# Optimization experiments

Measured on AMD Instinct MI355X. Metric: run time of the kernel, lower is better.

## Reference

```python
import jax, jax.numpy as jnp
import numpy as np

HIDDEN = 256
HEADS = 4
N_CHECKINS = 500000
N_POIS = 50000


def setup_inputs() -> dict:
    key = jax.random.key(0)
    ks = jax.random.split(key, 12)
    lim = 1.0 / np.sqrt(HIDDEN)
    def lin(k):
        kw, kb = jax.random.split(k)
        W = jax.random.uniform(kw, (HIDDEN, HIDDEN), jnp.float32, -lim, lim)
        b = jax.random.uniform(kb, (HIDDEN,), jnp.float32, -lim, lim)
        return W, b
    Wq, bq = lin(ks[0]); Wk, bk = lin(ks[1]); Wv, bv = lin(ks[2]); Wo, bo = lin(ks[3])
    # xavier_uniform for S [1, hidden]: gain=1, fan_in=hidden, fan_out=1
    a = np.sqrt(6.0 / (HIDDEN + 1))
    S = jax.random.uniform(ks[4], (1, HIDDEN), jnp.float32, -a, a)
    prelu_a = jnp.float32(0.25)  # PReLU default init
    x = jax.random.normal(ks[5], (N_CHECKINS, HIDDEN), jnp.float32)
    checkin_to_poi = jax.random.randint(ks[6], (N_CHECKINS,), 0, N_POIS, jnp.int64 if jax.config.jax_enable_x64 else jnp.int32)
    return {"x": x, "checkin_to_poi": checkin_to_poi, "num_pois": N_POIS,
            "Wq": Wq, "bq": bq, "Wk": Wk, "bk": bk, "Wv": Wv, "bv": bv,
            "Wo": Wo, "bo": bo, "S": S, "prelu_a": prelu_a}


def reference(x, checkin_to_poi, num_pois, Wq, bq, Wk, bk, Wv, bv, Wo, bo, S, prelu_a):
    C = x.shape[1]
    H = HEADS
    d = C // H
    idx = checkin_to_poi
    K = x @ Wk.T + bk                      # [N, C]
    V = x @ Wv.T + bv                      # [N, C]
    Q = S @ Wq.T + bq                      # [1, C]
    Ks = K.reshape(-1, H, d)
    Vs = V.reshape(-1, H, d)
    Qs = Q.reshape(1, H, d)
    scale = jnp.sqrt(jnp.float32(C))
    scores = (Ks * Qs).sum(-1) / scale     # [N, H]
    # segment softmax over POI groups (pyg_softmax)
    smax = jax.ops.segment_max(scores, idx, num_segments=num_pois)  # [P, H]
    smax = jnp.where(jnp.isfinite(smax), smax, 0.0)  # empty segments -> -inf -> 0
    e = jnp.exp(scores - smax[idx])
    denom = jax.ops.segment_sum(e, idx, num_segments=num_pois)      # [P, H]
    alpha = e / (denom[idx] + 1e-16)       # [N, H]
    weighted_V = Vs * alpha[..., None]     # [N, H, d]
    poi_agg = jax.ops.segment_sum(weighted_V.reshape(-1, C), idx, num_segments=num_pois)  # [P, C]
    O = Q + poi_agg                        # broadcast Q over POIs
    O = O + jax.nn.relu(O @ Wo.T + bo)
    O = jnp.where(O >= 0, O, prelu_a * O)  # PReLU (single shared parameter)
    return jnp.nan_to_num(O, nan=0.0)
```

## Files before the change

kernel.cpp:

```cpp
#include <hip/hip_runtime.h>
#include <stdint.h>

typedef __bf16 bf16x8 __attribute__((ext_vector_type(8)));
typedef float f32x4 __attribute__((ext_vector_type(4)));

#define MFMA16(A, B, C) __builtin_amdgcn_mfma_f32_16x16x32_bf16((A), (B), (C), 0, 0, 0)

__device__ __forceinline__ float b2f(unsigned short u) {
    union { unsigned int i; float f; } v; v.i = ((unsigned int)u) << 16; return v.f;
}
__device__ __forceinline__ unsigned short f2b(float f) {
    union { float f; unsigned int i; } v; v.f = f;
    unsigned int x = v.i;
    return (unsigned short)((x + 0x7FFFu + ((x >> 16) & 1u)) >> 16);
}
__device__ __forceinline__ float ldf(const void* p, long i, int isbf) {
    return isbf ? b2f(((const unsigned short*)p)[i]) : ((const float*)p)[i];
}

__global__ void k_probe(const unsigned int* __restrict__ wq,
                        const unsigned int* __restrict__ idxw, int* __restrict__ flags) {
    if (threadIdx.x == 0) {
        int ok = 0;
        for (int i = 0; i < 8; i++) {
            unsigned int e = (wq[i] >> 7) & 0xFFu;
            if (e >= 0x60u && e <= 0x7Cu) ok++;
        }
        flags[0] = (ok == 8) ? 1 : 0;
        int z = 0, lr = 0;
        for (int i = 0; i < 4; i++) {
            if (idxw[2 * i + 1] == 0u) z++;
            if (idxw[2 * i] < 0x4000000u) lr++;
        }
        flags[1] = (z == 4 && lr == 4) ? 1 : 0;
    }
}

__global__ void k_q(const void* __restrict__ S, const void* __restrict__ Wq,
                    const void* __restrict__ bq, const void* __restrict__ prelu,
                    const int* __restrict__ flags, float* __restrict__ Q,
                    float* __restrict__ pf) {
    int isbf = flags[0];
    int c = threadIdx.x;
    float acc = 0.f;
    for (int j = 0; j < 256; j++) acc += ldf(S, j, isbf) * ldf(Wq, (long)c * 256 + j, isbf);
    Q[c] = acc + ldf(bq, c, isbf);
    if (c == 0)
        pf[0] = isbf ? b2f(((const unsigned short*)prelu)[0]) : ((const float*)prelu)[0];
}

__global__ void k_qk(const void* __restrict__ Wk, const void* __restrict__ bk,
                     const float* __restrict__ Q, const int* __restrict__ flags,
                     unsigned short* __restrict__ qkb, float* __restrict__ qb) {
    int isbf = flags[0];
    int h = blockIdx.x, j = threadIdx.x;
    float acc = 0.f;
    if (h < 4) {
        for (int d = 0; d < 64; d++) acc += ldf(Wk, (long)(h * 64 + d) * 256 + j, isbf) * Q[h * 64 + d];
        acc *= 0.0625f;
    }
    qkb[h * 256 + j] = f2b(acc);
    if (j == 0) {
        float s = 0.f;
        if (h < 4) {
            for (int d = 0; d < 64; d++) s += ldf(bk, h * 64 + d, isbf) * Q[h * 64 + d];
            s *= 0.0625f;
        }
        qb[h] = s;
    }
}

__global__ void k_cvt(const void* __restrict__ Wv, const void* __restrict__ Wo,
                      const int* __restrict__ flags, unsigned short* __restrict__ Wvb,
                      unsigned short* __restrict__ Wob) {
    int isbf = flags[0];
    long i = (long)blockIdx.x * 256 + threadIdx.x;
    const void* src = (i < 65536) ? Wv : Wo;
    unsigned short* dst = (i < 65536) ? Wvb : Wob;
    long k = (i < 65536) ? i : i - 65536;
    dst[k] = isbf ? ((const unsigned short*)src)[k] : f2b(((const float*)src)[k]);
}

__global__ __launch_bounds__(256) void k_v(
    const void* __restrict__ x, const int* __restrict__ idxp,
    const unsigned short* __restrict__ Wvb, const unsigned short* __restrict__ qkb,
    const float* __restrict__ qb, const int* __restrict__ flags,
    float* __restrict__ denom, float* __restrict__ vagg, int N) {
    __shared__ unsigned short xs[128 * 264];
    __shared__ float es[128][4];
    int isbf = flags[0], is64 = flags[1];
    int tid = threadIdx.x;
    long base = (long)blockIdx.x * 128;

#pragma unroll
    for (int ch = 0; ch < 16; ch++) {
        int i16 = tid + ch * 256;
        int row = i16 >> 5;
        int col = (i16 & 31) * 8;
        long grow = base + row;
        uint4 t;
        if (grow < N) {
            if (isbf) {
                t = *(const uint4*)((const unsigned short*)x + grow * 256 + col);
            } else {
                const float* xp = (const float*)x + grow * 256 + col;
                float4 a = *(const float4*)xp;
                float4 b = *(const float4*)(xp + 4);
                t.x = (unsigned int)f2b(a.x) | ((unsigned int)f2b(a.y) << 16);
                t.y = (unsigned int)f2b(a.z) | ((unsigned int)f2b(a.w) << 16);
                t.z = (unsigned int)f2b(b.x) | ((unsigned int)f2b(b.y) << 16);
                t.w = (unsigned int)f2b(b.z) | ((unsigned int)f2b(b.w) << 16);
            }
        } else {
            t.x = t.y = t.z = t.w = 0u;
        }
        *(uint4*)&xs[row * 264 + col] = t;
    }
    __syncthreads();

    int w = tid >> 6, l = tid & 63;
    int m = l & 15, q = l >> 4;

    int ids[2][4];
#pragma unroll
    for (int g2 = 0; g2 < 2; g2++)
#pragma unroll
        for (int r = 0; r < 4; r++) {
            long gr = base + w * 32 + g2 * 16 + q * 4 + r;
            ids[g2][r] = (gr < N) ? (is64 ? idxp[gr << 1] : idxp[gr]) : 0;
        }

    bf16x8 a[2][8];
#pragma unroll
    for (int g2 = 0; g2 < 2; g2++)
#pragma unroll
        for (int s = 0; s < 8; s++)
            a[g2][s] = *(const bf16x8*)&xs[(w * 32 + g2 * 16 + m) * 264 + q * 8 + s * 32];

    {
        const bf16x8* qkp = (const bf16x8*)(qkb + (size_t)m * 256);
        bf16x8 qf[8];
#pragma unroll
        for (int s = 0; s < 8; s++) qf[s] = qkp[q + s * 4];
        float qbm = qb[m & 3];
#pragma unroll
        for (int g2 = 0; g2 < 2; g2++) {
            f32x4 sacc = {0.f, 0.f, 0.f, 0.f};
#pragma unroll
            for (int s = 0; s < 8; s++) sacc = MFMA16(a[g2][s], qf[s], sacc);
            if (m < 4) {
#pragma unroll
                for (int r = 0; r < 4; r++) {
                    int row = w * 32 + g2 * 16 + q * 4 + r;
                    long gr = base + row;
                    float e = 0.f;
                    if (gr < N) {
                        e = __expf(sacc[r] + qbm);
                        unsafeAtomicAdd(&denom[(long)ids[g2][r] * 4 + m], e);
                    }
                    es[row][m] = e;
                }
            }
        }
    }

#pragma unroll 1
    for (int t = 0; t < 16; t++) {
        int h_t = t >> 2;
        const bf16x8* wvp = (const bf16x8*)(Wvb + (size_t)(t * 16 + m) * 256);
        bf16x8 b[8];
#pragma unroll
        for (int s = 0; s < 8; s++) b[s] = wvp[q + s * 4];
#pragma unroll
        for (int g2 = 0; g2 < 2; g2++) {
            f32x4 acc = {0.f, 0.f, 0.f, 0.f};
#pragma unroll
            for (int s = 0; s < 8; s++) acc = MFMA16(a[g2][s], b[s], acc);
#pragma unroll
            for (int r = 0; r < 4; r++) {
                int row = w * 32 + g2 * 16 + q * 4 + r;
                long gr = base + row;
                if (gr < N) {
                    float val = acc[r] * es[row][h_t];
                    unsafeAtomicAdd(&vagg[(long)ids[g2][r] * 256 + t * 16 + m], val);
                }
            }
        }
    }
}

__global__ __launch_bounds__(256) void k_out(
    const float* __restrict__ Q, const float* __restrict__ denom,
    const float* __restrict__ vagg, const void* __restrict__ bv,
    const unsigned short* __restrict__ Wob, const void* __restrict__ bo,
    const float* __restrict__ pf, const int* __restrict__ flags,
    void* __restrict__ out, int P) {
    __shared__ float Os[4][16 * 264];
    int isbf = flags[0];
    int tid = threadIdx.x;
    int w = tid >> 6, l = tid & 63;
    int m = l & 15, q = l >> 4;
    long pbase = (long)blockIdx.x * 64 + w * 16;
    float aP = pf[0];
    long pm = pbase + m;
    bool vm = pm < P;

    float den4[4], rd4[4];
#pragma unroll
    for (int h = 0; h < 4; h++) {
        float d = vm ? denom[pm * 4 + h] : 0.f;
        den4[h] = d;
        rd4[h] = 1.0f / (d + 1e-16f);
    }

    bf16x8 of[8];
#pragma unroll
    for (int s = 0; s < 8; s++) {
        int c0 = q * 8 + s * 32;
        int h = s >> 1;
        bf16x8 ov;
        if (vm) {
            const float* ag = vagg + pm * 256 + c0;
#pragma unroll
            for (int j = 0; j < 8; j++) {
                float o = Q[c0 + j] + (ag[j] + ldf(bv, c0 + j, isbf) * den4[h]) * rd4[h];
                Os[w][m * 264 + c0 + j] = o;
                ov[j] = (__bf16)o;
            }
        } else {
#pragma unroll
            for (int j = 0; j < 8; j++) { Os[w][m * 264 + c0 + j] = 0.f; ov[j] = (__bf16)0.0f; }
        }
        of[s] = ov;
    }

#pragma unroll 1
    for (int t = 0; t < 16; t++) {
        const bf16x8* wop = (const bf16x8*)(Wob + (size_t)(t * 16 + m) * 256);
        f32x4 acc = {0.f, 0.f, 0.f, 0.f};
#pragma unroll
        for (int s = 0; s < 8; s++) acc = MFMA16(of[s], wop[q + s * 4], acc);
        int c = t * 16 + m;
        float boc = ldf(bo, c, isbf);
#pragma unroll
        for (int r = 0; r < 4; r++) {
            int row = q * 4 + r;
            long p = pbase + row;
            if (p < P) {
                float Ov = Os[w][row * 264 + c];
                float lin = fmaxf(acc[r] + boc, 0.f);
                float res = Ov + lin;
                res = (res >= 0.f) ? res : aP * res;
                if (res != res) res = 0.f;
                if (isbf) ((unsigned short*)out)[p * 256 + c] = f2b(res);
                else      ((float*)out)[p * 256 + c] = res;
            }
        }
    }
}

extern "C" void kernel_launch(void* const* d_in, const int* in_sizes, int n_in,
                              void* d_out, int out_size, void* d_ws, size_t ws_size,
                              hipStream_t stream) {
    const void* x  = d_in[0];
    const int* idx = (const int*)d_in[1];
    const void* Wq = d_in[3];
    const void* bq = d_in[4];
    const void* Wk = d_in[5];
    const void* bk = d_in[6];
    const void* Wv = d_in[7];
    const void* bv = d_in[8];
    const void* Wo = d_in[9];
    const void* bo = d_in[10];
    const void* S  = d_in[11];
    const void* pr = d_in[12];

    int N = in_sizes[0] / 256;
    int P = out_size / 256;

    float* ws = (float*)d_ws;
    int* flags          = (int*)ws;
    float* pf           = ws + 2;
    float* Q            = ws + 16;
    float* qb           = ws + 272;
    unsigned short* qkb = (unsigned short*)(ws + 288);
    unsigned short* Wvb = (unsigned short*)(ws + 2336);
    unsigned short* Wob = (unsigned short*)(ws + 35104);
    float* denom        = ws + 67872;
    float* vagg         = denom + (size_t)P * 4;

    size_t need = (67872 + (size_t)P * 260) * sizeof(float);
    if (ws_size < need) return;

    hipMemsetAsync(denom, 0, (size_t)P * 260 * sizeof(float), stream);

    k_probe<<<1, 64, 0, stream>>>((const unsigned int*)Wq, (const unsigned int*)idx, flags);
    k_q<<<1, 256, 0, stream>>>(S, Wq, bq, pr, flags, Q, pf);
    k_qk<<<16, 256, 0, stream>>>(Wk, bk, Q, flags, qkb, qb);
    k_cvt<<<512, 256, 0, stream>>>(Wv, Wo, flags, Wvb, Wob);
    k_v<<<(N + 127) / 128, 256, 0, stream>>>(x, idx, Wvb, qkb, qb, flags, denom, vagg, N);
    k_out<<<(P + 63) / 64, 256, 0, stream>>>(Q, denom, vagg, bv, Wob, bo, pf, flags, d_out, P);
}
```

Measured before the change: 1.238 ms.

## Sort checkins by POI via counting sort and coalesce atomics per segment

New measurement: 1.260 ms. No clear change (+1.7%).

```diff
diff --git a/kernel.cpp b/kernel.cpp
--- a/kernel.cpp
+++ b/kernel.cpp
@@ -81,14 +81,93 @@
     dst[k] = isbf ? ((const unsigned short*)src)[k] : f2b(((const float*)src)[k]);
 }
 
+
+__global__ void k_hist(const int* __restrict__ idxp, const int* __restrict__ flags,
+                       int* __restrict__ counts, int N) {
+    int is64 = flags[1];
+    int i = blockIdx.x * 256 + threadIdx.x;
+    if (i < N) {
+        int p = is64 ? idxp[(long)i << 1] : idxp[i];
+        atomicAdd(&counts[p], 1);
+    }
+}
+
+__global__ __launch_bounds__(256) void k_scan1(const int* __restrict__ counts,
+                                               int* __restrict__ offs,
+                                               int* __restrict__ bsum, int P) {
+    __shared__ int sh[256];
+    int t = threadIdx.x;
+    int i = blockIdx.x * 256 + t;
+    int v = (i < P) ? counts[i] : 0;
+    int s = v;
+    sh[t] = s;
+    __syncthreads();
+    for (int d = 1; d < 256; d <<= 1) {
+        int add = (t >= d) ? sh[t - d] : 0;
+        __syncthreads();
+        s += add;
+        sh[t] = s;
+        __syncthreads();
+    }
+    if (i < P) offs[i] = s - v;
+    if (t == 255) bsum[blockIdx.x] = s;
+}
+
+__global__ __launch_bounds__(256) void k_scan2(int* __restrict__ bsum, int nb) {
+    __shared__ int sh[256];
+    int t = threadIdx.x;
+    int K = (nb + 255) / 256;
+    int j0 = t * K;
+    int local = 0;
+    for (int k = 0; k < K; k++) {
+        int j = j0 + k;
+        if (j < nb) local += bsum[j];
+    }
+    int s = local;
+    sh[t] = s;
+    __syncthreads();
+    for (int d = 1; d < 256; d <<= 1) {
+        int add = (t >= d) ? sh[t - d] : 0;
+        __syncthreads();
+        s += add;
+        sh[t] = s;
+        __syncthreads();
+    }
+    int run = s - local;
+    for (int k = 0; k < K; k++) {
+        int j = j0 + k;
+        if (j < nb) { int tmp = bsum[j]; bsum[j] = run; run += tmp; }
+    }
+}
+
+__global__ void k_scan3(int* __restrict__ offs, const int* __restrict__ bsum, int P) {
+    int i = blockIdx.x * 256 + threadIdx.x;
+    if (i < P) offs[i] += bsum[blockIdx.x];
+}
+
+__global__ void k_scatter(const int* __restrict__ idxp, const int* __restrict__ flags,
+                          const int* __restrict__ offs, int* __restrict__ cursor,
+                          int* __restrict__ order, int* __restrict__ pois, int N) {
+    int is64 = flags[1];
+    int i = blockIdx.x * 256 + threadIdx.x;
+    if (i < N) {
+        int p = is64 ? idxp[(long)i << 1] : idxp[i];
+        int pos = atomicAdd(&cursor[p], 1);
+        int j = offs[p] + pos;
+        order[j] = i;
+        pois[j] = p;
+    }
+}
+
 __global__ __launch_bounds__(256) void k_v(
-    const void* __restrict__ x, const int* __restrict__ idxp,
+    const void* __restrict__ x, const int* __restrict__ order,
+    const int* __restrict__ pois,
     const unsigned short* __restrict__ Wvb, const unsigned short* __restrict__ qkb,
     const float* __restrict__ qb, const int* __restrict__ flags,
     float* __restrict__ denom, float* __restrict__ vagg, int N) {
     __shared__ unsigned short xs[128 * 264];
     __shared__ float es[128][4];
-    int isbf = flags[0], is64 = flags[1];
+    int isbf = flags[0];
     int tid = threadIdx.x;
     long base = (long)blockIdx.x * 128;
 
@@ -100,10 +179,11 @@
         long grow = base + row;
         uint4 t;
         if (grow < N) {
+            long n = (long)order[grow];
             if (isbf) {
-                t = *(const uint4*)((const unsigned short*)x + grow * 256 + col);
+                t = *(const uint4*)((const unsigned short*)x + n * 256 + col);
             } else {
-                const float* xp = (const float*)x + grow * 256 + col;
+                const float* xp = (const float*)x + n * 256 + col;
                 float4 a = *(const float4*)xp;
                 float4 b = *(const float4*)(xp + 4);
                 t.x = (unsigned int)f2b(a.x) | ((unsigned int)f2b(a.y) << 16);
@@ -127,7 +207,7 @@
 #pragma unroll
         for (int r = 0; r < 4; r++) {
             long gr = base + w * 32 + g2 * 16 + q * 4 + r;
-            ids[g2][r] = (gr < N) ? (is64 ? idxp[gr << 1] : idxp[gr]) : 0;
+            ids[g2][r] = (gr < N) ? pois[gr] : -1;
         }
 
     bf16x8 a[2][8];
@@ -149,17 +229,25 @@
 #pragma unroll
             for (int s = 0; s < 8; s++) sacc = MFMA16(a[g2][s], qf[s], sacc);
             if (m < 4) {
+                int rid = -1;
+                float run = 0.f;
 #pragma unroll
                 for (int r = 0; r < 4; r++) {
                     int row = w * 32 + g2 * 16 + q * 4 + r;
                     long gr = base + row;
                     float e = 0.f;
-                    if (gr < N) {
-                        e = __expf(sacc[r] + qbm);
-                        unsafeAtomicAdd(&denom[(long)ids[g2][r] * 4 + m], e);
+                    if (gr < N) e = __expf(sacc[r] + qbm);
+                    es[row][m] = e;
+                    int id = ids[g2][r];
+                    if (id == rid) {
+                        run += e;
+                    } else {
+                        if (rid >= 0) unsafeAtomicAdd(&denom[(long)rid * 4 + m], run);
+                        rid = id;
+                        run = e;
                     }
-                    es[row][m] = e;
                 }
+                if (rid >= 0) unsafeAtomicAdd(&denom[(long)rid * 4 + m], run);
             }
         }
     }
@@ -176,15 +264,22 @@
             f32x4 acc = {0.f, 0.f, 0.f, 0.f};
 #pragma unroll
             for (int s = 0; s < 8; s++) acc = MFMA16(a[g2][s], b[s], acc);
+            int rid = -1;
+            float run = 0.f;
 #pragma unroll
             for (int r = 0; r < 4; r++) {
                 int row = w * 32 + g2 * 16 + q * 4 + r;
-                long gr = base + row;
-                if (gr < N) {
-                    float val = acc[r] * es[row][h_t];
-                    unsafeAtomicAdd(&vagg[(long)ids[g2][r] * 256 + t * 16 + m], val);
+                float val = acc[r] * es[row][h_t];
+                int id = ids[g2][r];
+                if (id == rid) {
+                    run += val;
+                } else {
+                    if (rid >= 0) unsafeAtomicAdd(&vagg[(long)rid * 256 + t * 16 + m], run);
+                    rid = id;
+                    run = val;
                 }
             }
+            if (rid >= 0) unsafeAtomicAdd(&vagg[(long)rid * 256 + t * 16 + m], run);
         }
     }
 }
@@ -277,6 +372,8 @@
 
     int N = in_sizes[0] / 256;
     int P = out_size / 256;
+    int nb1 = (P + 255) / 256;
+    int nbN = (N + 255) / 256;
 
     float* ws = (float*)d_ws;
     int* flags          = (int*)ws;
@@ -289,15 +386,32 @@
     float* denom        = ws + 67872;
     float* vagg         = denom + (size_t)P * 4;
 
-    size_t need = (67872 + (size_t)P * 260) * sizeof(float);
+    int* counts = (int*)vagg;
+    int* cursor = counts + P;
+    int* offs   = cursor + P;
+    int* bsum   = offs + P;
+
+    int* order  = (int*)(vagg + (size_t)P * 256);
+    int* pois   = order + N;
+
+    size_t need = (67872 + (size_t)P * 260) * sizeof(float) + (size_t)2 * N * sizeof(int);
     if (ws_size < need) return;
 
-    hipMemsetAsync(denom, 0, (size_t)P * 260 * sizeof(float), stream);
+    hipMemsetAsync(counts, 0, (size_t)2 * P * sizeof(int), stream);
 
     k_probe<<<1, 64, 0, stream>>>((const unsigned int*)Wq, (const unsigned int*)idx, flags);
     k_q<<<1, 256, 0, stream>>>(S, Wq, bq, pr, flags, Q, pf);
     k_qk<<<16, 256, 0, stream>>>(Wk, bk, Q, flags, qkb, qb);
     k_cvt<<<512, 256, 0, stream>>>(Wv, Wo, flags, Wvb, Wob);
-    k_v<<<(N + 127) / 128, 256, 0, stream>>>(x, idx, Wvb, qkb, qb, flags, denom, vagg, N);
+
+    k_hist<<<nbN, 256, 0, stream>>>(idx, flags, counts, N);
+    k_scan1<<<nb1, 256, 0, stream>>>(counts, offs, bsum, P);
+    k_scan2<<<1, 256, 0, stream>>>(bsum, nb1);
+    k_scan3<<<nb1, 256, 0, stream>>>(offs, bsum, P);
+    k_scatter<<<nbN, 256, 0, stream>>>(idx, flags, offs, cursor, order, pois, N);
+
+    hipMemsetAsync(denom, 0, (size_t)P * 260 * sizeof(float), stream);
+
+    k_v<<<(N + 127) / 128, 256, 0, stream>>>(x, order, pois, Wvb, qkb, qb, flags, denom, vagg, N);
     k_out<<<(P + 63) / 64, 256, 0, stream>>>(Q, denom, vagg, bv, Wob, bo, pf, flags, d_out, P);
 }
```
